# Performance work log

Measured on AMD Instinct MI355X. Metric: run time of the kernel, lower is better.

## Reference

```python
import jax, jax.numpy as jnp
import numpy as np

TOP_K = 2
NUM_EXPERTS = 8

def setup_inputs() -> dict:
    key = jax.random.key(0)
    k_x, k_r, k_g, k_u, k_d = jax.random.split(key, 5)
    B, L, D, H, E = 1, 2048, 1024, 2048, NUM_EXPERTS
    scale = 0.02  # keep router logits / activations in a sane range
    return {
        "x": jax.random.normal(k_x, (B, L, D), dtype=jnp.float32),
        "router_w": jax.random.normal(k_r, (D, E), dtype=jnp.float32) * scale,
        "gate_w": jax.random.normal(k_g, (E, D, H), dtype=jnp.float32) * scale,
        "up_w": jax.random.normal(k_u, (E, D, H), dtype=jnp.float32) * scale,
        "down_w": jax.random.normal(k_d, (E, H, D), dtype=jnp.float32) * scale,
    }

def reference(x, router_w, gate_w, up_w, down_w):
    # x: (B, L, D)
    B, L, D = x.shape
    T = B * L
    E = router_w.shape[1]
    xf = x.reshape(T, D)

    # --- router: top-k softmax over selected logits (Mixtral-style) ---
    logits = xf @ router_w                      # (T, E)
    top_vals, top_idx = jax.lax.top_k(logits, TOP_K)  # (T, K)
    top_w = jax.nn.softmax(top_vals, axis=-1)   # (T, K)

    # combine weights scattered to dense (T, E); zeros for unrouted experts
    combine = jnp.zeros((T, E), dtype=x.dtype).at[
        jnp.arange(T)[:, None], top_idx
    ].add(top_w)

    # --- experts: SwiGLU, computed per expert, zero-weight tokens masked by combine ---
    gate = jnp.einsum('td,edh->eth', xf, gate_w)   # (E, T, H)
    up = jnp.einsum('td,edh->eth', xf, up_w)       # (E, T, H)
    hidden = jax.nn.silu(gate) * up                # (E, T, H)
    expert_out = jnp.einsum('eth,ehd->etd', hidden, down_w)  # (E, T, D)

    # --- weighted combine (equivalent to scatter_add over sorted assignments) ---
    y = jnp.einsum('etd,te->td', expert_out, combine)  # (T, D)
    return y.reshape(B, L, D)
```

## Files before the change

kernel.cpp:

```cpp
#include <hip/hip_runtime.h>
#include <hip/hip_bf16.h>
#include <stdint.h>

#define T_TOK 2048
#define DIM   1024
#define HDIM  2048
#define NE    8
#define ROWS_PAD 4224
#define TSLOTS 40

typedef __attribute__((ext_vector_type(8))) short bf16x8;
typedef __attribute__((ext_vector_type(8))) unsigned short u16x8;
typedef __attribute__((ext_vector_type(4))) float f32x4;
typedef __attribute__((ext_vector_type(4))) unsigned int u32x4;

__device__ __forceinline__ unsigned short f2bf(float f) {
    union { __hip_bfloat16 h; unsigned short u; } cv;
    cv.h = __float2bfloat16(f);
    return cv.u;
}
__device__ __forceinline__ unsigned int f2bf2(float lo, float hi) {
    union { __hip_bfloat162 h; unsigned int u; } cv;
    cv.h = __float22bfloat162_rn(make_float2(lo, hi));
    return cv.u;
}
__device__ __forceinline__ float bf2f(unsigned short b) {
    union { unsigned int u; float f; } v; v.u = ((unsigned int)b) << 16;
    return v.f;
}

__device__ __forceinline__ void gload16(const void* g, void* l) {
    __builtin_amdgcn_global_load_lds(
        (const __attribute__((address_space(1))) void*)g,
        (__attribute__((address_space(3))) void*)l, 16, 0, 0);
}

__global__ void router_kernel(const float* __restrict__ x, const float* __restrict__ rw,
                              int* __restrict__ counts, int* __restrict__ top_idx,
                              float* __restrict__ top_w) {
    int wid = (blockIdx.x * blockDim.x + threadIdx.x) >> 6;
    int lane = threadIdx.x & 63;
    if (wid >= T_TOK) return;
    float acc[NE];
#pragma unroll
    for (int e = 0; e < NE; ++e) acc[e] = 0.f;
    const float* xr = x + (size_t)wid * DIM;
    for (int i = lane; i < DIM; i += 64) {
        float xv = xr[i];
        const float* wr = rw + (size_t)i * NE;
#pragma unroll
        for (int e = 0; e < NE; ++e) acc[e] += xv * wr[e];
    }
#pragma unroll
    for (int off = 32; off; off >>= 1) {
#pragma unroll
        for (int e = 0; e < NE; ++e) acc[e] += __shfl_xor(acc[e], off, 64);
    }
    if (lane == 0) {
        float v0 = -1e30f, v1 = -1e30f; int i0 = 0, i1 = 0;
#pragma unroll
        for (int e = 0; e < NE; ++e) {
            float v = acc[e];
            if (v > v0) { v1 = v0; i1 = i0; v0 = v; i0 = e; }
            else if (v > v1) { v1 = v; i1 = e; }
        }
        float e1 = __expf(v1 - v0);
        float s = 1.f + e1;
        top_idx[wid * 2]     = i0;
        top_idx[wid * 2 + 1] = i1;
        top_w[wid * 2]     = 1.f / s;
        top_w[wid * 2 + 1] = e1 / s;
        atomicAdd(&counts[i0], 1);
        atomicAdd(&counts[i1], 1);
    }
}

__global__ void scan_kernel(const int* __restrict__ counts, int* __restrict__ offsets,
                            int* __restrict__ cursors,
                            int* __restrict__ tl_e, int* __restrict__ tl_m) {
    if (threadIdx.x == 0) {
        int run = 0;
        for (int e = 0; e < NE; ++e) { offsets[e] = run; cursors[e] = run; run += counts[e]; }
        int n = 0;
        for (int e = 0; e < NE; ++e) {
            int mt = (counts[e] + 127) >> 7;
            for (int m = 0; m < mt && n < 64; ++m) { tl_e[n] = e; tl_m[n] = m; ++n; }
        }
        for (; n < 64; ++n) tl_e[n] = -1;
    }
}

__global__ void gather_kernel(const float* __restrict__ x, const int* __restrict__ top_idx,
                              const float* __restrict__ top_w, int* __restrict__ cursors,
                              int* __restrict__ row_tok, float* __restrict__ row_w,
                              unsigned short* __restrict__ Abuf) {
    int t = blockIdx.x;
    __shared__ int pos[2];
    if (threadIdx.x < 2) {
        int k = threadIdx.x;
        int e = top_idx[t * 2 + k];
        int p = atomicAdd(&cursors[e], 1);
        pos[k] = p;
        row_tok[p] = t;
        row_w[p] = top_w[t * 2 + k];
    }
    __syncthreads();
    const float4* xr = (const float4*)(x + (size_t)t * DIM);
    float4 v = xr[threadIdx.x];
    uint2 b; b.x = f2bf2(v.x, v.y); b.y = f2bf2(v.z, v.w);
    uint2* A4 = (uint2*)Abuf;
    A4[(size_t)pos[0] * (DIM / 4) + threadIdx.x] = b;
    A4[(size_t)pos[1] * (DIM / 4) + threadIdx.x] = b;
}

__global__ __launch_bounds__(256, 3)
void gemm1s_kernel(const unsigned short* __restrict__ Abuf,
                   const float* __restrict__ gw,
                   const float* __restrict__ uw,
                   unsigned short* __restrict__ Hs,
                   unsigned short* __restrict__ Hu,
                   const int* __restrict__ offsets, const int* __restrict__ counts,
                   const int* __restrict__ tl_e, const int* __restrict__ tl_m) {
    const int slot = blockIdx.y;
    const int e = tl_e[slot];
    if (e < 0) return;
    const int mtile = tl_m[slot];
    const int cnt = counts[e];
    const int n0 = blockIdx.x * 64;
    const int row0 = offsets[e] + mtile * 128;
    const int zu = blockIdx.z;
    const float* W = zu ? uw : gw;
    unsigned short* Hx = zu ? Hu : Hs;

    __shared__ unsigned short AsB[2][128 * 64];
    __shared__ unsigned short Bb[2][64 * 64];

    const int tid = threadIdx.x;
    const int lane = tid & 63;
    const int wave = tid >> 6;
    const int wm = wave >> 1;
    const int wn = wave & 1;

    f32x4 acc[4][2];
#pragma unroll
    for (int i = 0; i < 4; ++i)
#pragma unroll
        for (int j = 0; j < 2; ++j) acc[i][j] = (f32x4){0.f, 0.f, 0.f, 0.f};

    const int srow = tid >> 3;
    const int sc0 = tid & 7;
    const unsigned short* Aab = Abuf + (size_t)row0 * DIM;

    auto stageA = [&](int buf, int kt) {
#pragma unroll
        for (int i = 0; i < 4; ++i) {
            int row = i * 32 + srow;
            int csrc = sc0 ^ (row & 7);
            gload16(Aab + (size_t)row * DIM + kt + csrc * 8,
                    &AsB[buf][(i * 256 + tid) * 8]);
        }
    };

    const int bn = tid & 63;
    const int bc0 = tid >> 6;
    const float* Bgb = W + (size_t)e * DIM * HDIM + n0 + bn;

    float bl[2][8];
    auto bload = [&](int kt) {
#pragma unroll
        for (int cc = 0; cc < 2; ++cc) {
            int c = bc0 + cc * 4;
            const float* gs = Bgb + (size_t)(kt + c * 8) * HDIM;
#pragma unroll
            for (int jj = 0; jj < 8; ++jj)
                bl[cc][jj] = gs[(size_t)jj * HDIM];
        }
    };
    auto bwrite = [&](int buf) {
#pragma unroll
        for (int cc = 0; cc < 2; ++cc) {
            int c = bc0 + cc * 4;
            int la = bn * 64 + ((c ^ (bn & 7)) * 8);
            u32x4 v;
#pragma unroll
            for (int p = 0; p < 4; ++p)
                v[p] = f2bf2(bl[cc][2 * p], bl[cc][2 * p + 1]);
            *(u32x4*)&Bb[buf][la] = v;
        }
    };

    const int rsel = lane & 15;
    const int csrcf = lane >> 4;

    stageA(0, 0);
    bload(0);
    bwrite(0);
    int cur = 0;
    for (int kt = 0; kt < DIM; kt += 64) {
        __syncthreads();
        const bool pre = (kt + 64 < DIM);
        if (pre) { stageA(cur ^ 1, kt + 64); bload(kt + 64); }
        const unsigned short* Ac = AsB[cur];
        const unsigned short* Bc = Bb[cur];
#pragma unroll
        for (int kk = 0; kk < 2; ++kk) {
            bf16x8 af[4], bb[2];
#pragma unroll
            for (int i = 0; i < 4; ++i) {
                int ra = wm * 64 + i * 16 + rsel;
                af[i] = *(const bf16x8*)&Ac[ra * 64 + ((kk * 4 + csrcf) ^ (ra & 7)) * 8];
            }
#pragma unroll
            for (int j = 0; j < 2; ++j) {
                int rb = wn * 32 + j * 16 + rsel;
                bb[j] = *(const bf16x8*)&Bc[rb * 64 + ((kk * 4 + csrcf) ^ (rb & 7)) * 8];
            }
#pragma unroll
            for (int i = 0; i < 4; ++i)
#pragma unroll
                for (int j = 0; j < 2; ++j)
                    acc[i][j] = __builtin_amdgcn_mfma_f32_16x16x32_bf16(af[i], bb[j], acc[i][j], 0, 0, 0);
        }
        if (pre) bwrite(cur ^ 1);
        cur ^= 1;
    }

    const int c = lane & 15, rbase = (lane >> 4) * 4;
    const int obase = offsets[e];
#pragma unroll
    for (int i = 0; i < 4; ++i) {
#pragma unroll
        for (int r = 0; r < 4; ++r) {
            int lrow = mtile * 128 + wm * 64 + i * 16 + rbase + r;
            if (lrow < cnt) {
                size_t orow = (size_t)(obase + lrow);
#pragma unroll
                for (int j = 0; j < 2; ++j) {
                    float v = acc[i][j][r];
                    if (!zu) v = v / (1.f + __expf(-v));
                    Hx[orow * HDIM + n0 + wn * 32 + j * 16 + c] = f2bf(v);
                }
            }
        }
    }
}

__global__ __launch_bounds__(256, 3)
void gemm2_kernel(const unsigned short* __restrict__ Hs,
                  const unsigned short* __restrict__ Hu,
                  const float* __restrict__ dw,
                  float* __restrict__ y,
                  const int* __restrict__ offsets, const int* __restrict__ counts,
                  const int* __restrict__ row_tok, const float* __restrict__ row_w,
                  const int* __restrict__ tl_e, const int* __restrict__ tl_m) {
    const int slot = blockIdx.y;
    const int e = tl_e[slot];
    if (e < 0) return;
    const int mtile = tl_m[slot];
    const int kc = blockIdx.z & 1;
    const int cnt = counts[e];
    const int n0 = blockIdx.x * 64;
    const int row0 = offsets[e] + mtile * 128;

    __shared__ unsigned short As[2][128 * 64];
    __shared__ unsigned short Bs[2][64 * 64];

    const int tid = threadIdx.x;
    const int lane = tid & 63;
    const int wave = tid >> 6;
    const int wm = wave >> 1, wn = wave & 1;

    f32x4 acc[4][2];
#pragma unroll
    for (int i = 0; i < 4; ++i)
#pragma unroll
        for (int j = 0; j < 2; ++j) acc[i][j] = (f32x4){0.f, 0.f, 0.f, 0.f};

    const int srow = tid >> 3;
    const int sc0 = tid & 7;
    const unsigned short* Asb = Hs + (size_t)row0 * HDIM;
    const unsigned short* Aub = Hu + (size_t)row0 * HDIM;

    u16x8 as_[4], au_[4];
    auto aload = [&](int kt) {
#pragma unroll
        for (int i = 0; i < 4; ++i) {
            int row = i * 32 + srow;
            size_t go = (size_t)row * HDIM + kt + sc0 * 8;
            as_[i] = *(const u16x8*)&Asb[go];
            au_[i] = *(const u16x8*)&Aub[go];
        }
    };
    auto awrite = [&](int buf) {
#pragma unroll
        for (int i = 0; i < 4; ++i) {
            int row = i * 32 + srow;
            int la = row * 64 + ((sc0 ^ (row & 7)) * 8);
            u32x4 v;
#pragma unroll
            for (int p = 0; p < 4; ++p) {
                float h0 = bf2f(as_[i][2 * p])     * bf2f(au_[i][2 * p]);
                float h1 = bf2f(as_[i][2 * p + 1]) * bf2f(au_[i][2 * p + 1]);
                v[p] = f2bf2(h0, h1);
            }
            *(u32x4*)&As[buf][la] = v;
        }
    };

    const int bn = tid & 63;
    const int bc0 = tid >> 6;
    const float* Bbb = dw + (size_t)e * HDIM * DIM + n0 + bn;

    float bl[2][8];
    auto bload = [&](int kt) {
#pragma unroll
        for (int cc = 0; cc < 2; ++cc) {
            int c = bc0 + cc * 4;
            const float* bs = Bbb + (size_t)(kt + c * 8) * DIM;
#pragma unroll
            for (int jj = 0; jj < 8; ++jj)
                bl[cc][jj] = bs[(size_t)jj * DIM];
        }
    };
    auto bwrite = [&](int buf) {
#pragma unroll
        for (int cc = 0; cc < 2; ++cc) {
            int c = bc0 + cc * 4;
            int la = bn * 64 + ((c ^ (bn & 7)) * 8);
            u32x4 v;
#pragma unroll
            for (int p = 0; p < 4; ++p)
                v[p] = f2bf2(bl[cc][2 * p], bl[cc][2 * p + 1]);
            *(u32x4*)&Bs[buf][la] = v;
        }
    };

    const int rsel = lane & 15;
    const int csrcf = lane >> 4;

    const int kbeg = kc * (HDIM / 2);
    const int kend = kbeg + (HDIM / 2);

    aload(kbeg);
    bload(kbeg);
    awrite(0);
    bwrite(0);
    int cur = 0;
    for (int kt = kbeg; kt < kend; kt += 64) {
        __syncthreads();
        const bool pre = (kt + 64 < kend);
        if (pre) { aload(kt + 64); bload(kt + 64); }
        const unsigned short* Ac = As[cur];
        const unsigned short* Bc = Bs[cur];
#pragma unroll
        for (int kk = 0; kk < 2; ++kk) {
            bf16x8 af[4], bf[2];
#pragma unroll
            for (int i = 0; i < 4; ++i) {
                int ra = wm * 64 + i * 16 + rsel;
                af[i] = *(const bf16x8*)&Ac[ra * 64 + ((kk * 4 + csrcf) ^ (ra & 7)) * 8];
            }
#pragma unroll
            for (int j = 0; j < 2; ++j) {
                int rb = wn * 32 + j * 16 + rsel;
                bf[j] = *(const bf16x8*)&Bc[rb * 64 + ((kk * 4 + csrcf) ^ (rb & 7)) * 8];
            }
#pragma unroll
            for (int i = 0; i < 4; ++i)
#pragma unroll
                for (int j = 0; j < 2; ++j)
                    acc[i][j] = __builtin_amdgcn_mfma_f32_16x16x32_bf16(af[i], bf[j], acc[i][j], 0, 0, 0);
        }
        if (pre) { awrite(cur ^ 1); bwrite(cur ^ 1); }
        cur ^= 1;
    }

    const int c = lane & 15, rbase = (lane >> 4) * 4;
    const int obase = offsets[e];
#pragma unroll
    for (int i = 0; i < 4; ++i) {
#pragma unroll
        for (int r = 0; r < 4; ++r) {
            int lrow = mtile * 128 + wm * 64 + i * 16 + rbase + r;
            if (lrow < cnt) {
                int grow = obase + lrow;
                int tok = row_tok[grow];
                float w = row_w[grow];
#pragma unroll
                for (int j = 0; j < 2; ++j) {
                    atomicAdd(&y[(size_t)tok * DIM + n0 + wn * 32 + j * 16 + c], w * acc[i][j][r]);
                }
            }
        }
    }
}

extern "C" void kernel_launch(void* const* d_in, const int* in_sizes, int n_in,
                              void* d_out, int out_size, void* d_ws, size_t ws_size,
                              hipStream_t stream) {
    const float* x  = (const float*)d_in[0];
    const float* rw = (const float*)d_in[1];
    const float* gw = (const float*)d_in[2];
    const float* uw = (const float*)d_in[3];
    const float* dw = (const float*)d_in[4];
    float* y = (float*)d_out;

    char* ws = (char*)d_ws;
    int*   counts  = (int*)(ws + 0);
    int*   cursors = (int*)(ws + 32);
    int*   offsets = (int*)(ws + 64);
    int*   top_idx = (int*)(ws + 128);
    float* top_w   = (float*)(ws + 128 + 16384);
    int*   row_tok = (int*)(ws + 128 + 32768);
    float* row_w   = (float*)(ws + 128 + 32768 + 16896);
    int*   tl_e    = (int*)(ws + 128 + 32768 + 2 * 16896);
    int*   tl_m    = (int*)(ws + 128 + 32768 + 2 * 16896 + 256);
    size_t off = 128 + 32768 + 2 * 16896 + 512;
    off = (off + 255) & ~(size_t)255;
    unsigned short* Abuf = (unsigned short*)(ws + off); off += (size_t)ROWS_PAD * DIM * 2;
    unsigned short* Hs   = (unsigned short*)(ws + off); off += (size_t)ROWS_PAD * HDIM * 2;
    unsigned short* Hu   = (unsigned short*)(ws + off); off += (size_t)ROWS_PAD * HDIM * 2;
    if (ws_size < off) return;

    hipMemsetAsync(counts, 0, 32, stream);
    hipMemsetAsync(d_out, 0, (size_t)out_size * 4, stream);

    router_kernel<<<T_TOK / 4, 256, 0, stream>>>(x, rw, counts, top_idx, top_w);
    scan_kernel<<<1, 64, 0, stream>>>(counts, offsets, cursors, tl_e, tl_m);
    gather_kernel<<<T_TOK, 256, 0, stream>>>(x, top_idx, top_w, cursors, row_tok, row_w, Abuf);

    gemm1s_kernel<<<dim3(HDIM / 64, TSLOTS, 2), 256, 0, stream>>>(Abuf, gw, uw, Hs, Hu,
                                                                  offsets, counts, tl_e, tl_m);
    gemm2_kernel<<<dim3(DIM / 64, TSLOTS, 2), 256, 0, stream>>>(Hs, Hu, dw, y, offsets, counts,
                                                                row_tok, row_w, tl_e, tl_m);
}
```

Measured before the change: 247.7 us.

## Drop LDS staging in expert GEMMs and load MFMA fragments directly from global

Both expert GEMM kernels no longer stage A and B tiles through shared memory with double buffering and barriers. Each wave now reads its MFMA fragments directly from global memory each K step, converting fp32 weights to bf16 in registers, and launch bounds are raised to allow four blocks per SM. This removes LDS traffic and __syncthreads but loses cross-wave reuse: tiles are fetched redundantly by each wave, and B loads are strided column reads with no software prefetch, which leaves more load latency exposed.

After: 453.6 us. 1.83x slower.

```diff
diff --git a/kernel.cpp b/kernel.cpp
--- a/kernel.cpp
+++ b/kernel.cpp
@@ -12,7 +12,6 @@
 typedef __attribute__((ext_vector_type(8))) short bf16x8;
 typedef __attribute__((ext_vector_type(8))) unsigned short u16x8;
 typedef __attribute__((ext_vector_type(4))) float f32x4;
-typedef __attribute__((ext_vector_type(4))) unsigned int u32x4;
 
 __device__ __forceinline__ unsigned short f2bf(float f) {
     union { __hip_bfloat16 h; unsigned short u; } cv;
@@ -27,12 +26,6 @@
 __device__ __forceinline__ float bf2f(unsigned short b) {
     union { unsigned int u; float f; } v; v.u = ((unsigned int)b) << 16;
     return v.f;
-}
-
-__device__ __forceinline__ void gload16(const void* g, void* l) {
-    __builtin_amdgcn_global_load_lds(
-        (const __attribute__((address_space(1))) void*)g,
-        (__attribute__((address_space(3))) void*)l, 16, 0, 0);
 }
 
 __global__ void router_kernel(const float* __restrict__ x, const float* __restrict__ rw,
@@ -113,8 +106,8 @@
     A4[(size_t)pos[1] * (DIM / 4) + threadIdx.x] = b;
 }
 
-__global__ __launch_bounds__(256, 3)
-void gemm1s_kernel(const unsigned short* __restrict__ Abuf,
+__global__ __launch_bounds__(256, 4)
+void gemm1z_kernel(const unsigned short* __restrict__ Abuf,
                    const float* __restrict__ gw,
                    const float* __restrict__ uw,
                    unsigned short* __restrict__ Hs,
@@ -132,97 +125,53 @@
     const float* W = zu ? uw : gw;
     unsigned short* Hx = zu ? Hu : Hs;
 
-    __shared__ unsigned short AsB[2][128 * 64];
-    __shared__ unsigned short Bb[2][64 * 64];
-
     const int tid = threadIdx.x;
     const int lane = tid & 63;
     const int wave = tid >> 6;
     const int wm = wave >> 1;
     const int wn = wave & 1;
 
+    const int rsel = lane & 15;
+    const int krd = (lane >> 4) * 8;
+
     f32x4 acc[4][2];
 #pragma unroll
     for (int i = 0; i < 4; ++i)
 #pragma unroll
         for (int j = 0; j < 2; ++j) acc[i][j] = (f32x4){0.f, 0.f, 0.f, 0.f};
 
-    const int srow = tid >> 3;
-    const int sc0 = tid & 7;
-    const unsigned short* Aab = Abuf + (size_t)row0 * DIM;
-
-    auto stageA = [&](int buf, int kt) {
-#pragma unroll
-        for (int i = 0; i < 4; ++i) {
-            int row = i * 32 + srow;
-            int csrc = sc0 ^ (row & 7);
-            gload16(Aab + (size_t)row * DIM + kt + csrc * 8,
-                    &AsB[buf][(i * 256 + tid) * 8]);
-        }
-    };
-
-    const int bn = tid & 63;
-    const int bc0 = tid >> 6;
-    const float* Bgb = W + (size_t)e * DIM * HDIM + n0 + bn;
-
-    float bl[2][8];
-    auto bload = [&](int kt) {
-#pragma unroll
-        for (int cc = 0; cc < 2; ++cc) {
-            int c = bc0 + cc * 4;
-            const float* gs = Bgb + (size_t)(kt + c * 8) * HDIM;
-#pragma unroll
-            for (int jj = 0; jj < 8; ++jj)
-                bl[cc][jj] = gs[(size_t)jj * HDIM];
-        }
-    };
-    auto bwrite = [&](int buf) {
-#pragma unroll
-        for (int cc = 0; cc < 2; ++cc) {
-            int c = bc0 + cc * 4;
-            int la = bn * 64 + ((c ^ (bn & 7)) * 8);
-            u32x4 v;
-#pragma unroll
-            for (int p = 0; p < 4; ++p)
-                v[p] = f2bf2(bl[cc][2 * p], bl[cc][2 * p + 1]);
-            *(u32x4*)&Bb[buf][la] = v;
-        }
-    };
-
-    const int rsel = lane & 15;
-    const int csrcf = lane >> 4;
-
-    stageA(0, 0);
-    bload(0);
-    bwrite(0);
-    int cur = 0;
-    for (int kt = 0; kt < DIM; kt += 64) {
-        __syncthreads();
-        const bool pre = (kt + 64 < DIM);
-        if (pre) { stageA(cur ^ 1, kt + 64); bload(kt + 64); }
-        const unsigned short* Ac = AsB[cur];
-        const unsigned short* Bc = Bb[cur];
-#pragma unroll
-        for (int kk = 0; kk < 2; ++kk) {
-            bf16x8 af[4], bb[2];
-#pragma unroll
-            for (int i = 0; i < 4; ++i) {
-                int ra = wm * 64 + i * 16 + rsel;
-                af[i] = *(const bf16x8*)&Ac[ra * 64 + ((kk * 4 + csrcf) ^ (ra & 7)) * 8];
-            }
-#pragma unroll
-            for (int j = 0; j < 2; ++j) {
-                int rb = wn * 32 + j * 16 + rsel;
-                bb[j] = *(const bf16x8*)&Bc[rb * 64 + ((kk * 4 + csrcf) ^ (rb & 7)) * 8];
-            }
-#pragma unroll
-            for (int i = 0; i < 4; ++i)
-#pragma unroll
-                for (int j = 0; j < 2; ++j)
-                    acc[i][j] = __builtin_amdgcn_mfma_f32_16x16x32_bf16(af[i], bb[j], acc[i][j], 0, 0, 0);
-        }
-        if (pre) bwrite(cur ^ 1);
-        cur ^= 1;
+    const unsigned short* Arow[4];
+#pragma unroll
+    for (int i = 0; i < 4; ++i)
+        Arow[i] = Abuf + (size_t)(row0 + wm * 64 + i * 16 + rsel) * DIM + krd;
+
+    const float* Bcol[2];
+#pragma unroll
+    for (int j = 0; j < 2; ++j)
+        Bcol[j] = W + (size_t)e * DIM * HDIM + (n0 + wn * 32 + j * 16 + rsel);
+
+    for (int kt = 0; kt < DIM; kt += 32) {
+        bf16x8 af[4];
+#pragma unroll
+        for (int i = 0; i < 4; ++i)
+            af[i] = *(const bf16x8*)(Arow[i] + kt);
+        bf16x8 bf[2];
+#pragma unroll
+        for (int j = 0; j < 2; ++j) {
+            const float* bp = Bcol[j] + (size_t)(kt + krd) * HDIM;
+            float v[8];
+#pragma unroll
+            for (int q = 0; q < 8; ++q) v[q] = bp[(size_t)q * HDIM];
+            union { unsigned int w[4]; bf16x8 h; } cv;
+#pragma unroll
+            for (int p = 0; p < 4; ++p) cv.w[p] = f2bf2(v[2 * p], v[2 * p + 1]);
+            bf[j] = cv.h;
+        }
+#pragma unroll
+        for (int i = 0; i < 4; ++i)
+#pragma unroll
+            for (int j = 0; j < 2; ++j)
+                acc[i][j] = __builtin_amdgcn_mfma_f32_16x16x32_bf16(af[i], bf[j], acc[i][j], 0, 0, 0);
     }
 
     const int c = lane & 15, rbase = (lane >> 4) * 4;
@@ -245,134 +194,86 @@
     }
 }
 
-__global__ __launch_bounds__(256, 3)
-void gemm2_kernel(const unsigned short* __restrict__ Hs,
-                  const unsigned short* __restrict__ Hu,
-                  const float* __restrict__ dw,
-                  float* __restrict__ y,
-                  const int* __restrict__ offsets, const int* __restrict__ counts,
-                  const int* __restrict__ row_tok, const float* __restrict__ row_w,
-                  const int* __restrict__ tl_e, const int* __restrict__ tl_m) {
+__global__ __launch_bounds__(256, 4)
+void gemm2z_kernel(const unsigned short* __restrict__ Hs,
+                   const unsigned short* __restrict__ Hu,
+                   const float* __restrict__ dw,
+                   float* __restrict__ y,
+                   const int* __restrict__ offsets, const int* __restrict__ counts,
+                   const int* __restrict__ row_tok, const float* __restrict__ row_w,
+                   const int* __restrict__ tl_e, const int* __restrict__ tl_m) {
     const int slot = blockIdx.y;
     const int e = tl_e[slot];
     if (e < 0) return;
     const int mtile = tl_m[slot];
-    const int kc = blockIdx.z & 1;
+    const int kc = blockIdx.z;
     const int cnt = counts[e];
     const int n0 = blockIdx.x * 64;
     const int row0 = offsets[e] + mtile * 128;
-
-    __shared__ unsigned short As[2][128 * 64];
-    __shared__ unsigned short Bs[2][64 * 64];
 
     const int tid = threadIdx.x;
     const int lane = tid & 63;
     const int wave = tid >> 6;
     const int wm = wave >> 1, wn = wave & 1;
 
+    const int rsel = lane & 15;
+    const int krd = (lane >> 4) * 8;
+
     f32x4 acc[4][2];
 #pragma unroll
     for (int i = 0; i < 4; ++i)
 #pragma unroll
         for (int j = 0; j < 2; ++j) acc[i][j] = (f32x4){0.f, 0.f, 0.f, 0.f};
 
-    const int srow = tid >> 3;
-    const int sc0 = tid & 7;
-    const unsigned short* Asb = Hs + (size_t)row0 * HDIM;
-    const unsigned short* Aub = Hu + (size_t)row0 * HDIM;
-
-    u16x8 as_[4], au_[4];
-    auto aload = [&](int kt) {
-#pragma unroll
-        for (int i = 0; i < 4; ++i) {
-            int row = i * 32 + srow;
-            size_t go = (size_t)row * HDIM + kt + sc0 * 8;
-            as_[i] = *(const u16x8*)&Asb[go];
-            au_[i] = *(const u16x8*)&Aub[go];
-        }
-    };
-    auto awrite = [&](int buf) {
-#pragma unroll
-        for (int i = 0; i < 4; ++i) {
-            int row = i * 32 + srow;
-            int la = row * 64 + ((sc0 ^ (row & 7)) * 8);
-            u32x4 v;
-#pragma unroll
-            for (int p = 0; p < 4; ++p) {
-                float h0 = bf2f(as_[i][2 * p])     * bf2f(au_[i][2 * p]);
-                float h1 = bf2f(as_[i][2 * p + 1]) * bf2f(au_[i][2 * p + 1]);
-                v[p] = f2bf2(h0, h1);
-            }
-            *(u32x4*)&As[buf][la] = v;
-        }
-    };
-
-    const int bn = tid & 63;
-    const int bc0 = tid >> 6;
-    const float* Bbb = dw + (size_t)e * HDIM * DIM + n0 + bn;
-
-    float bl[2][8];
-    auto bload = [&](int kt) {
-#pragma unroll
-        for (int cc = 0; cc < 2; ++cc) {
-            int c = bc0 + cc * 4;
-            const float* bs = Bbb + (size_t)(kt + c * 8) * DIM;
-#pragma unroll
-            for (int jj = 0; jj < 8; ++jj)
-                bl[cc][jj] = bs[(size_t)jj * DIM];
-        }
-    };
-    auto bwrite = [&](int buf) {
-#pragma unroll
-        for (int cc = 0; cc < 2; ++cc) {
-            int c = bc0 + cc * 4;
-            int la = bn * 64 + ((c ^ (bn & 7)) * 8);
-            u32x4 v;
-#pragma unroll
-            for (int p = 0; p < 4; ++p)
-                v[p] = f2bf2(bl[cc][2 * p], bl[cc][2 * p + 1]);
-            *(u32x4*)&Bs[buf][la] = v;
-        }
-    };
-
-    const int rsel = lane & 15;
-    const int csrcf = lane >> 4;
+    const unsigned short* Asrow[4];
+    const unsigned short* Aurow[4];
+#pragma unroll
+    for (int i = 0; i < 4; ++i) {
+        size_t ro = (size_t)(row0 + wm * 64 + i * 16 + rsel) * HDIM + krd;
+        Asrow[i] = Hs + ro;
+        Aurow[i] = Hu + ro;
+    }
+
+    const float* Bcol[2];
+#pragma unroll
+    for (int j = 0; j < 2; ++j)
+        Bcol[j] = dw + (size_t)e * HDIM * DIM + (n0 + wn * 32 + j * 16 + rsel);
 
     const int kbeg = kc * (HDIM / 2);
     const int kend = kbeg + (HDIM / 2);
 
-    aload(kbeg);
-    bload(kbeg);
-    awrite(0);
-    bwrite(0);
-    int cur = 0;
-    for (int kt = kbeg; kt < kend; kt += 64) {
-        __syncthreads();
-        const bool pre = (kt + 64 < kend);
-        if (pre) { aload(kt + 64); bload(kt + 64); }
-        const unsigned short* Ac = As[cur];
-        const unsigned short* Bc = Bs[cur];
-#pragma unroll
-        for (int kk = 0; kk < 2; ++kk) {
-            bf16x8 af[4], bf[2];
-#pragma unroll
-            for (int i = 0; i < 4; ++i) {
-                int ra = wm * 64 + i * 16 + rsel;
-                af[i] = *(const bf16x8*)&Ac[ra * 64 + ((kk * 4 + csrcf) ^ (ra & 7)) * 8];
+    for (int kt = kbeg; kt < kend; kt += 32) {
+        bf16x8 af[4];
+#pragma unroll
+        for (int i = 0; i < 4; ++i) {
+            u16x8 s8 = *(const u16x8*)(Asrow[i] + kt);
+            u16x8 u8 = *(const u16x8*)(Aurow[i] + kt);
+            union { unsigned int w[4]; bf16x8 h; } cv;
+#pragma unroll
+            for (int p = 0; p < 4; ++p) {
+                float h0 = bf2f(s8[2 * p])     * bf2f(u8[2 * p]);
+                float h1 = bf2f(s8[2 * p + 1]) * bf2f(u8[2 * p + 1]);
+                cv.w[p] = f2bf2(h0, h1);
             }
-#pragma unroll
-            for (int j = 0; j < 2; ++j) {
-                int rb = wn * 32 + j * 16 + rsel;
-                bf[j] = *(const bf16x8*)&Bc[rb * 64 + ((kk * 4 + csrcf) ^ (rb & 7)) * 8];
-            }
-#pragma unroll
-            for (int i = 0; i < 4; ++i)
-#pragma unroll
-                for (int j = 0; j < 2; ++j)
-                    acc[i][j] = __builtin_amdgcn_mfma_f32_16x16x32_bf16(af[i], bf[j], acc[i][j], 0, 0, 0);
-        }
-        if (pre) { awrite(cur ^ 1); bwrite(cur ^ 1); }
-        cur ^= 1;
+            af[i] = cv.h;
+        }
+        bf16x8 bf[2];
+#pragma unroll
+        for (int j = 0; j < 2; ++j) {
+            const float* bp = Bcol[j] + (size_t)(kt + krd) * DIM;
+            float v[8];
+#pragma unroll
+            for (int q = 0; q < 8; ++q) v[q] = bp[(size_t)q * DIM];
+            union { unsigned int w[4]; bf16x8 h; } cv;
+#pragma unroll
+            for (int p = 0; p < 4; ++p) cv.w[p] = f2bf2(v[2 * p], v[2 * p + 1]);
+            bf[j] = cv.h;
+        }
+#pragma unroll
+        for (int i = 0; i < 4; ++i)
+#pragma unroll
+            for (int j = 0; j < 2; ++j)
+                acc[i][j] = __builtin_amdgcn_mfma_f32_16x16x32_bf16(af[i], bf[j], acc[i][j], 0, 0, 0);
     }
 
     const int c = lane & 15, rbase = (lane >> 4) * 4;
@@ -429,8 +330,8 @@
     scan_kernel<<<1, 64, 0, stream>>>(counts, offsets, cursors, tl_e, tl_m);
     gather_kernel<<<T_TOK, 256, 0, stream>>>(x, top_idx, top_w, cursors, row_tok, row_w, Abuf);
 
-    gemm1s_kernel<<<dim3(HDIM / 64, TSLOTS, 2), 256, 0, stream>>>(Abuf, gw, uw, Hs, Hu,
+    gemm1z_kernel<<<dim3(HDIM / 64, TSLOTS, 2), 256, 0, stream>>>(Abuf, gw, uw, Hs, Hu,
                                                                   offsets, counts, tl_e, tl_m);
-    gemm2_kernel<<<dim3(DIM / 64, TSLOTS, 2), 256, 0, stream>>>(Hs, Hu, dw, y, offsets, counts,
-                                                                row_tok, row_w, tl_e, tl_m);
-}
+    gemm2z_kernel<<<dim3(DIM / 64, TSLOTS, 2), 256, 0, stream>>>(Hs, Hu, dw, y, offsets, counts,
+                                                                 row_tok, row_w, tl_e, tl_m);
+}
```

## Shrink expert GEMM tiles to 64 rows with 2-wave blocks and drop split-K

Applied to the files above, without the earlier changes.

Both expert GEMMs move from 128-row, 4-wave tiles to 64-row, 2-wave tiles, and the tile list grows to 80 slots. The goal is less padding waste per expert and more blocks in flight. The fp32 weight loads change from strided scalar reads to float4 row reads, which are then transposed in registers before the bf16 write to shared memory. The down-projection GEMM no longer splits K in two, so each output gets one atomic add instead of two, at the cost of fewer parallel blocks and each weight tile being re-read by twice as many row tiles.

Result: slower. 300.5 us (+21.3%).

```diff
diff --git a/kernel.cpp b/kernel.cpp
--- a/kernel.cpp
+++ b/kernel.cpp
@@ -7,7 +7,7 @@
 #define HDIM  2048
 #define NE    8
 #define ROWS_PAD 4224
-#define TSLOTS 40
+#define TS64 80
 
 typedef __attribute__((ext_vector_type(8))) short bf16x8;
 typedef __attribute__((ext_vector_type(8))) unsigned short u16x8;
@@ -83,10 +83,10 @@
         for (int e = 0; e < NE; ++e) { offsets[e] = run; cursors[e] = run; run += counts[e]; }
         int n = 0;
         for (int e = 0; e < NE; ++e) {
-            int mt = (counts[e] + 127) >> 7;
-            for (int m = 0; m < mt && n < 64; ++m) { tl_e[n] = e; tl_m[n] = m; ++n; }
-        }
-        for (; n < 64; ++n) tl_e[n] = -1;
+            int mt = (counts[e] + 63) >> 6;
+            for (int m = 0; m < mt && n < TS64; ++m) { tl_e[n] = e; tl_m[n] = m; ++n; }
+        }
+        for (; n < TS64; ++n) tl_e[n] = -1;
     }
 }
 
@@ -113,7 +113,7 @@
     A4[(size_t)pos[1] * (DIM / 4) + threadIdx.x] = b;
 }
 
-__global__ __launch_bounds__(256, 3)
+__global__ __launch_bounds__(128, 2)
 void gemm1s_kernel(const unsigned short* __restrict__ Abuf,
                    const float* __restrict__ gw,
                    const float* __restrict__ uw,
@@ -127,19 +127,17 @@
     const int mtile = tl_m[slot];
     const int cnt = counts[e];
     const int n0 = blockIdx.x * 64;
-    const int row0 = offsets[e] + mtile * 128;
+    const int row0 = offsets[e] + mtile * 64;
     const int zu = blockIdx.z;
     const float* W = zu ? uw : gw;
     unsigned short* Hx = zu ? Hu : Hs;
 
-    __shared__ unsigned short AsB[2][128 * 64];
+    __shared__ unsigned short AsB[2][64 * 64];
     __shared__ unsigned short Bb[2][64 * 64];
 
     const int tid = threadIdx.x;
     const int lane = tid & 63;
-    const int wave = tid >> 6;
-    const int wm = wave >> 1;
-    const int wn = wave & 1;
+    const int wn = tid >> 6;
 
     f32x4 acc[4][2];
 #pragma unroll
@@ -147,45 +145,40 @@
 #pragma unroll
         for (int j = 0; j < 2; ++j) acc[i][j] = (f32x4){0.f, 0.f, 0.f, 0.f};
 
-    const int srow = tid >> 3;
-    const int sc0 = tid & 7;
     const unsigned short* Aab = Abuf + (size_t)row0 * DIM;
-
     auto stageA = [&](int buf, int kt) {
 #pragma unroll
         for (int i = 0; i < 4; ++i) {
-            int row = i * 32 + srow;
-            int csrc = sc0 ^ (row & 7);
+            int idx = i * 128 + tid;
+            int row = idx >> 3, sc = idx & 7;
+            int csrc = sc ^ (row & 7);
             gload16(Aab + (size_t)row * DIM + kt + csrc * 8,
-                    &AsB[buf][(i * 256 + tid) * 8]);
-        }
-    };
-
-    const int bn = tid & 63;
-    const int bc0 = tid >> 6;
-    const float* Bgb = W + (size_t)e * DIM * HDIM + n0 + bn;
-
-    float bl[2][8];
+                    &AsB[buf][idx * 8]);
+        }
+    };
+
+    const int nq = tid & 15;
+    const int kc = tid >> 4;
+    const float* Bgb = W + (size_t)e * DIM * HDIM + n0 + nq * 4;
+
+    float4 bl[8];
     auto bload = [&](int kt) {
 #pragma unroll
-        for (int cc = 0; cc < 2; ++cc) {
-            int c = bc0 + cc * 4;
-            const float* gs = Bgb + (size_t)(kt + c * 8) * HDIM;
-#pragma unroll
-            for (int jj = 0; jj < 8; ++jj)
-                bl[cc][jj] = gs[(size_t)jj * HDIM];
-        }
+        for (int kk = 0; kk < 8; ++kk)
+            bl[kk] = *(const float4*)&Bgb[(size_t)(kt + kc * 8 + kk) * HDIM];
     };
     auto bwrite = [&](int buf) {
 #pragma unroll
-        for (int cc = 0; cc < 2; ++cc) {
-            int c = bc0 + cc * 4;
-            int la = bn * 64 + ((c ^ (bn & 7)) * 8);
-            u32x4 v;
-#pragma unroll
-            for (int p = 0; p < 4; ++p)
-                v[p] = f2bf2(bl[cc][2 * p], bl[cc][2 * p + 1]);
-            *(u32x4*)&Bb[buf][la] = v;
+        for (int q = 0; q < 4; ++q) {
+            int c = nq * 4 + q;
+            float v[8];
+#pragma unroll
+            for (int kk = 0; kk < 8; ++kk)
+                v[kk] = (q == 0) ? bl[kk].x : (q == 1) ? bl[kk].y : (q == 2) ? bl[kk].z : bl[kk].w;
+            u32x4 h;
+#pragma unroll
+            for (int p = 0; p < 4; ++p) h[p] = f2bf2(v[2 * p], v[2 * p + 1]);
+            *(u32x4*)&Bb[buf][c * 64 + ((kc ^ (c & 7)) * 8)] = h;
         }
     };
 
@@ -207,7 +200,7 @@
             bf16x8 af[4], bb[2];
 #pragma unroll
             for (int i = 0; i < 4; ++i) {
-                int ra = wm * 64 + i * 16 + rsel;
+                int ra = i * 16 + rsel;
                 af[i] = *(const bf16x8*)&Ac[ra * 64 + ((kk * 4 + csrcf) ^ (ra & 7)) * 8];
             }
 #pragma unroll
@@ -231,7 +224,7 @@
     for (int i = 0; i < 4; ++i) {
 #pragma unroll
         for (int r = 0; r < 4; ++r) {
-            int lrow = mtile * 128 + wm * 64 + i * 16 + rbase + r;
+            int lrow = mtile * 64 + i * 16 + rbase + r;
             if (lrow < cnt) {
                 size_t orow = (size_t)(obase + lrow);
 #pragma unroll
@@ -245,30 +238,28 @@
     }
 }
 
-__global__ __launch_bounds__(256, 3)
-void gemm2_kernel(const unsigned short* __restrict__ Hs,
-                  const unsigned short* __restrict__ Hu,
-                  const float* __restrict__ dw,
-                  float* __restrict__ y,
-                  const int* __restrict__ offsets, const int* __restrict__ counts,
-                  const int* __restrict__ row_tok, const float* __restrict__ row_w,
-                  const int* __restrict__ tl_e, const int* __restrict__ tl_m) {
+__global__ __launch_bounds__(128, 2)
+void gemm2s_kernel(const unsigned short* __restrict__ Hs,
+                   const unsigned short* __restrict__ Hu,
+                   const float* __restrict__ dw,
+                   float* __restrict__ y,
+                   const int* __restrict__ offsets, const int* __restrict__ counts,
+                   const int* __restrict__ row_tok, const float* __restrict__ row_w,
+                   const int* __restrict__ tl_e, const int* __restrict__ tl_m) {
     const int slot = blockIdx.y;
     const int e = tl_e[slot];
     if (e < 0) return;
     const int mtile = tl_m[slot];
-    const int kc = blockIdx.z & 1;
     const int cnt = counts[e];
     const int n0 = blockIdx.x * 64;
-    const int row0 = offsets[e] + mtile * 128;
-
-    __shared__ unsigned short As[2][128 * 64];
+    const int row0 = offsets[e] + mtile * 64;
+
+    __shared__ unsigned short As[2][64 * 64];
     __shared__ unsigned short Bs[2][64 * 64];
 
     const int tid = threadIdx.x;
     const int lane = tid & 63;
-    const int wave = tid >> 6;
-    const int wm = wave >> 1, wn = wave & 1;
+    const int wn = tid >> 6;
 
     f32x4 acc[4][2];
 #pragma unroll
@@ -276,79 +267,71 @@
 #pragma unroll
         for (int j = 0; j < 2; ++j) acc[i][j] = (f32x4){0.f, 0.f, 0.f, 0.f};
 
-    const int srow = tid >> 3;
-    const int sc0 = tid & 7;
-    const unsigned short* Asb = Hs + (size_t)row0 * HDIM;
-    const unsigned short* Aub = Hu + (size_t)row0 * HDIM;
+    const int ar = tid >> 1;
+    const int ah = (tid & 1) * 4;
+    const unsigned short* Asb = Hs + (size_t)(row0 + ar) * HDIM;
+    const unsigned short* Aub = Hu + (size_t)(row0 + ar) * HDIM;
 
     u16x8 as_[4], au_[4];
     auto aload = [&](int kt) {
 #pragma unroll
-        for (int i = 0; i < 4; ++i) {
-            int row = i * 32 + srow;
-            size_t go = (size_t)row * HDIM + kt + sc0 * 8;
-            as_[i] = *(const u16x8*)&Asb[go];
-            au_[i] = *(const u16x8*)&Aub[go];
+        for (int cc = 0; cc < 4; ++cc) {
+            size_t go = (size_t)kt + (ah + cc) * 8;
+            as_[cc] = *(const u16x8*)&Asb[go];
+            au_[cc] = *(const u16x8*)&Aub[go];
         }
     };
     auto awrite = [&](int buf) {
 #pragma unroll
-        for (int i = 0; i < 4; ++i) {
-            int row = i * 32 + srow;
-            int la = row * 64 + ((sc0 ^ (row & 7)) * 8);
+        for (int cc = 0; cc < 4; ++cc) {
+            int ch = ah + cc;
             u32x4 v;
 #pragma unroll
             for (int p = 0; p < 4; ++p) {
-                float h0 = bf2f(as_[i][2 * p])     * bf2f(au_[i][2 * p]);
-                float h1 = bf2f(as_[i][2 * p + 1]) * bf2f(au_[i][2 * p + 1]);
+                float h0 = bf2f(as_[cc][2 * p])     * bf2f(au_[cc][2 * p]);
+                float h1 = bf2f(as_[cc][2 * p + 1]) * bf2f(au_[cc][2 * p + 1]);
                 v[p] = f2bf2(h0, h1);
             }
-            *(u32x4*)&As[buf][la] = v;
-        }
-    };
-
-    const int bn = tid & 63;
-    const int bc0 = tid >> 6;
-    const float* Bbb = dw + (size_t)e * HDIM * DIM + n0 + bn;
-
-    float bl[2][8];
+            *(u32x4*)&As[buf][ar * 64 + ((ch ^ (ar & 7)) * 8)] = v;
+        }
+    };
+
+    const int nq = tid & 15;
+    const int kc = tid >> 4;
+    const float* Bbb = dw + (size_t)e * HDIM * DIM + n0 + nq * 4;
+
+    float4 bl[8];
     auto bload = [&](int kt) {
 #pragma unroll
-        for (int cc = 0; cc < 2; ++cc) {
-            int c = bc0 + cc * 4;
-            const float* bs = Bbb + (size_t)(kt + c * 8) * DIM;
-#pragma unroll
-            for (int jj = 0; jj < 8; ++jj)
-                bl[cc][jj] = bs[(size_t)jj * DIM];
-        }
+        for (int kk = 0; kk < 8; ++kk)
+            bl[kk] = *(const float4*)&Bbb[(size_t)(kt + kc * 8 + kk) * DIM];
     };
     auto bwrite = [&](int buf) {
 #pragma unroll
-        for (int cc = 0; cc < 2; ++cc) {
-            int c = bc0 + cc * 4;
-            int la = bn * 64 + ((c ^ (bn & 7)) * 8);
-            u32x4 v;
-#pragma unroll
-            for (int p = 0; p < 4; ++p)
-                v[p] = f2bf2(bl[cc][2 * p], bl[cc][2 * p + 1]);
-            *(u32x4*)&Bs[buf][la] = v;
+        for (int q = 0; q < 4; ++q) {
+            int c = nq * 4 + q;
+            float v[8];
+#pragma unroll
+            for (int kk = 0; kk < 8; ++kk)
+                v[kk] = (q == 0) ? bl[kk].x : (q == 1) ? bl[kk].y : (q == 2) ? bl[kk].z : bl[kk].w;
+            u32x4 h;
+#pragma unroll
+            for (int p = 0; p < 4; ++p) h[p] = f2bf2(v[2 * p], v[2 * p + 1]);
+            *(u32x4*)&Bs[buf][c * 64 + ((kc ^ (c & 7)) * 8)] = h;
         }
     };
 
     const int rsel = lane & 15;
     const int csrcf = lane >> 4;
 
-    const int kbeg = kc * (HDIM / 2);
-    const int kend = kbeg + (HDIM / 2);
-
-    aload(kbeg);
-    bload(kbeg);
+    aload(0);
+    bload(0);
     awrite(0);
     bwrite(0);
     int cur = 0;
-    for (int kt = kbeg; kt < kend; kt += 64) {
+    for (int kt = 0; kt < HDIM; kt += 64) {
         __syncthreads();
-        const bool pre = (kt + 64 < kend);
+        const bool pre = (kt + 64 < HDIM);
         if (pre) { aload(kt + 64); bload(kt + 64); }
         const unsigned short* Ac = As[cur];
         const unsigned short* Bc = Bs[cur];
@@ -357,7 +340,7 @@
             bf16x8 af[4], bf[2];
 #pragma unroll
             for (int i = 0; i < 4; ++i) {
-                int ra = wm * 64 + i * 16 + rsel;
+                int ra = i * 16 + rsel;
                 af[i] = *(const bf16x8*)&Ac[ra * 64 + ((kk * 4 + csrcf) ^ (ra & 7)) * 8];
             }
 #pragma unroll
@@ -381,7 +364,7 @@
     for (int i = 0; i < 4; ++i) {
 #pragma unroll
         for (int r = 0; r < 4; ++r) {
-            int lrow = mtile * 128 + wm * 64 + i * 16 + rbase + r;
+            int lrow = mtile * 64 + i * 16 + rbase + r;
             if (lrow < cnt) {
                 int grow = obase + lrow;
                 int tok = row_tok[grow];
@@ -414,8 +397,8 @@
     int*   row_tok = (int*)(ws + 128 + 32768);
     float* row_w   = (float*)(ws + 128 + 32768 + 16896);
     int*   tl_e    = (int*)(ws + 128 + 32768 + 2 * 16896);
-    int*   tl_m    = (int*)(ws + 128 + 32768 + 2 * 16896 + 256);
-    size_t off = 128 + 32768 + 2 * 16896 + 512;
+    int*   tl_m    = (int*)(ws + 128 + 32768 + 2 * 16896 + 512);
+    size_t off = 128 + 32768 + 2 * 16896 + 1024;
     off = (off + 255) & ~(size_t)255;
     unsigned short* Abuf = (unsigned short*)(ws + off); off += (size_t)ROWS_PAD * DIM * 2;
     unsigned short* Hs   = (unsigned short*)(ws + off); off += (size_t)ROWS_PAD * HDIM * 2;
@@ -429,8 +412,8 @@
     scan_kernel<<<1, 64, 0, stream>>>(counts, offsets, cursors, tl_e, tl_m);
     gather_kernel<<<T_TOK, 256, 0, stream>>>(x, top_idx, top_w, cursors, row_tok, row_w, Abuf);
 
-    gemm1s_kernel<<<dim3(HDIM / 64, TSLOTS, 2), 256, 0, stream>>>(Abuf, gw, uw, Hs, Hu,
-                                                                  offsets, counts, tl_e, tl_m);
-    gemm2_kernel<<<dim3(DIM / 64, TSLOTS, 2), 256, 0, stream>>>(Hs, Hu, dw, y, offsets, counts,
-                                                                row_tok, row_w, tl_e, tl_m);
-}
+    gemm1s_kernel<<<dim3(HDIM / 64, TS64, 2), 128, 0, stream>>>(Abuf, gw, uw, Hs, Hu,
+                                                                offsets, counts, tl_e, tl_m);
+    gemm2s_kernel<<<dim3(DIM / 64, TS64), 128, 0, stream>>>(Hs, Hu, dw, y, offsets, counts,
+                                                            row_tok, row_w, tl_e, tl_m);
+}
```
